# Kernel optimization log

Measured on AMD Instinct MI355X. Metric: run time of the kernel, lower is better.

## Reference

```python
import jax, jax.numpy as jnp
import numpy as np

B, N, C = 32, 577, 768
H = 12
D = C // H


def setup_inputs() -> dict:
    key = jax.random.key(0)
    ks = jax.random.split(key, 4)
    x = jax.random.normal(ks[0], (B, N, C), dtype=jnp.float32)
    w_qkv = jax.random.normal(ks[1], (C, 3 * C), dtype=jnp.float32) * (C ** -0.5)
    b_qkv = jnp.zeros((3 * C,), dtype=jnp.float32)
    # per-head learnable scale, initialized to head_dim**-0.5 scaled ones
    scale = jnp.ones((H,), dtype=jnp.float32) * (D ** -0.5)
    w_proj = jax.random.normal(ks[2], (C, C), dtype=jnp.float32) * (C ** -0.5)
    b_proj = jnp.zeros((C,), dtype=jnp.float32)
    return {"x": x, "w_qkv": w_qkv, "b_qkv": b_qkv, "scale": scale,
            "w_proj": w_proj, "b_proj": b_proj}


def reference(x, w_qkv, b_qkv, scale, w_proj, b_proj):
    b, n, c = x.shape
    h = scale.shape[0]
    d = c // h
    # fused QKV projection -> [b, n, 3, h, d]
    qkv = (x @ w_qkv + b_qkv).reshape(b, n, 3, h, d)
    q = qkv[:, :, 0]  # [b, n, h, d]
    k = qkv[:, :, 1]
    v = qkv[:, :, 2]
    # attention logits with per-head scale
    attn = jnp.einsum('bihd,bjhd->bhij', q, k) * scale[None, :, None, None]
    # custom mask: block self-attention among patch tokens (rows/cols 1:),
    # CLS token (index 0) unaffected
    if n > 1:
        mask = jnp.zeros((n, n), dtype=bool).at[1:, 1:].set(
            jnp.eye(n - 1, dtype=bool))
        attn = jnp.where(mask[None, None], -jnp.inf, attn)
    attn = jax.nn.softmax(attn, axis=-1)
    out = jnp.einsum('bhij,bjhd->bihd', attn, v).reshape(b, n, c)
    return out @ w_proj + b_proj
```

## Files before the change

### kernel.cpp

```cpp
#include <hip/hip_runtime.h>
#include <math.h>

#define HD 64
#define KVBLK 64
#define LP 72

typedef __attribute__((ext_vector_type(8))) short short8;
typedef __attribute__((ext_vector_type(4))) short short4v;
typedef __attribute__((ext_vector_type(4))) float f32x4;

__device__ __forceinline__ short f2bf(float f) {
    union { float f; unsigned u; } in;
    in.f = f;
    unsigned r = (in.u + 0x7fff + ((in.u >> 16) & 1)) >> 16;
    return (short)r;
}

__global__ __launch_bounds__(256) void convert_bf16(const float* __restrict__ in,
                                                    short* __restrict__ out, long n4) {
    long i = blockIdx.x * 256L + threadIdx.x;
    if (i >= n4) return;
    float4 v = reinterpret_cast<const float4*>(in)[i];
    short4v o;
    o[0] = f2bf(v.x); o[1] = f2bf(v.y); o[2] = f2bf(v.z); o[3] = f2bf(v.w);
    reinterpret_cast<short4v*>(out)[i] = o;
}

__global__ __launch_bounds__(256) void transpose_bf16(const float* __restrict__ in,
                                                      short* __restrict__ out, int K, int N) {
    __shared__ float tile[32][33];
    const int n0 = blockIdx.x * 32, k0 = blockIdx.y * 32;
    const int tx = threadIdx.x & 31, ty = threadIdx.x >> 5;
    #pragma unroll
    for (int i = ty; i < 32; i += 8)
        tile[i][tx] = in[(size_t)(k0 + i) * N + n0 + tx];
    __syncthreads();
    #pragma unroll
    for (int i = ty; i < 32; i += 8)
        out[(size_t)(n0 + i) * K + k0 + tx] = f2bf(tile[tx][i]);
}

__global__ __launch_bounds__(256) void transpose_v(const short* __restrict__ qkvb,
                                                   short* __restrict__ vT) {
    constexpr int Nn = 577, C3 = 2304, NH = 12, NKP = 640;
    const int bh = blockIdx.x;
    const int kt = blockIdx.y;
    const int b = bh / NH, h = bh % NH;
    const int tid = threadIdx.x;
    __shared__ short tile[64][33];

    const int tk = tid >> 3;
    const int key = kt * 32 + tk;
    const int d0 = (tid & 7) * 8;
    short8 v = {0, 0, 0, 0, 0, 0, 0, 0};
    if (key < Nn)
        v = *reinterpret_cast<const short8*>(
            qkvb + (size_t)(b * Nn + key) * C3 + 1536 + h * 64 + d0);
    #pragma unroll
    for (int i = 0; i < 8; ++i) tile[d0 + i][tk] = v[i];
    __syncthreads();

    const int d = tid >> 2;
    const int kb = (tid & 3) * 8;
    short8 o;
    #pragma unroll
    for (int i = 0; i < 8; ++i) o[i] = tile[d][kb + i];
    *reinterpret_cast<short8*>(vT + (size_t)(bh * 64 + d) * NKP + kt * 32 + kb) = o;
}

template <typename OutT>
__global__ __launch_bounds__(256, 2) void gemm_bf16(const short* __restrict__ A,
                                                    const short* __restrict__ Bt,
                                                    const float* __restrict__ bias,
                                                    OutT* __restrict__ C,
                                                    int M, int N, int K, int nbn) {
    __shared__ short As[2][128 * 64];
    __shared__ short Bs[2][64 * 64];
    const int tid = threadIdx.x;
    const int w = tid >> 6, lane = tid & 63;
    const int g = lane >> 4, l16 = lane & 15;

    const int nwg = gridDim.x;
    const int q = nwg >> 3, r = nwg & 7;
    const int xcd = blockIdx.x & 7, loc = blockIdx.x >> 3;
    const int wgid = (xcd < r ? xcd * (q + 1) : r * (q + 1) + (xcd - r) * q) + loc;
    const int bm = wgid / nbn, bn = wgid % nbn;
    const int m0 = bm * 256, n0 = bn * 128;
    const int wm = (w >> 1) * 128, wn = (w & 1) * 64;

    f32x4 acc[8][4] = {};
    const int NT = K >> 5;

    auto stage = [&](int buf, int k0) {
        #pragma unroll
        for (int j = 0; j < 4; ++j) {
            const int o = j * 4096 + tid * 16;
            const int R = o >> 7;
            const int sl = ((o >> 4) & 7) ^ (R & 7);
            const int rr = 2 * R + (sl >> 2);
            const int cblk = sl & 3;
            long arow = m0 + rr; if (arow > M - 1) arow = M - 1;
            const short* ga = A + arow * K + k0 + cblk * 8;
            __builtin_amdgcn_global_load_lds(
                (const __attribute__((address_space(1))) unsigned*)ga,
                (__attribute__((address_space(3))) unsigned*)((char*)&As[buf][0] + o),
                16, 0, 0);
        }
        #pragma unroll
        for (int j = 0; j < 2; ++j) {
            const int o = j * 4096 + tid * 16;
            const int R = o >> 7;
            const int sl = ((o >> 4) & 7) ^ (R & 7);
            const int rr = 2 * R + (sl >> 2);
            const int cblk = sl & 3;
            const short* gb = Bt + (size_t)(n0 + rr) * K + k0 + cblk * 8;
            __builtin_amdgcn_global_load_lds(
                (const __attribute__((address_space(1))) unsigned*)gb,
                (__attribute__((address_space(3))) unsigned*)((char*)&Bs[buf][0] + o),
                16, 0, 0);
        }
    };

    stage(0, 0);
    __syncthreads();

    for (int kt = 0; kt < NT; ++kt) {
        const int cur = kt & 1;
        if (kt + 1 < NT) stage(cur ^ 1, (kt + 1) * 32);

        short8 af[8], bfr[4];
        #pragma unroll
        for (int mi = 0; mi < 8; ++mi) {
            const int ra = wm + mi * 16 + l16;
            const int Ra = ra >> 1;
            const int sla = (4 * (ra & 1) + g) ^ (Ra & 7);
            af[mi] = *reinterpret_cast<const short8*>(&As[cur][Ra * 64 + sla * 8]);
        }
        #pragma unroll
        for (int ni = 0; ni < 4; ++ni) {
            const int rb = wn + ni * 16 + l16;
            const int Rb = rb >> 1;
            const int slb = (4 * (rb & 1) + g) ^ (Rb & 7);
            bfr[ni] = *reinterpret_cast<const short8*>(&Bs[cur][Rb * 64 + slb * 8]);
        }
        __builtin_amdgcn_s_setprio(1);
        #pragma unroll
        for (int mi = 0; mi < 8; ++mi)
            #pragma unroll
            for (int ni = 0; ni < 4; ++ni)
                acc[mi][ni] = __builtin_amdgcn_mfma_f32_16x16x32_bf16(
                    af[mi], bfr[ni], acc[mi][ni], 0, 0, 0);
        __builtin_amdgcn_s_setprio(0);
        __syncthreads();
    }

    float bv[4];
    #pragma unroll
    for (int ni = 0; ni < 4; ++ni) bv[ni] = bias[n0 + wn + ni * 16 + l16];
    #pragma unroll
    for (int mi = 0; mi < 8; ++mi) {
        #pragma unroll
        for (int rr = 0; rr < 4; ++rr) {
            const int row = m0 + wm + mi * 16 + g * 4 + rr;
            if (row < M) {
                #pragma unroll
                for (int ni = 0; ni < 4; ++ni) {
                    float val = acc[mi][ni][rr] + bv[ni];
                    if constexpr (__is_same(OutT, float))
                        C[(size_t)row * N + n0 + wn + ni * 16 + l16] = val;
                    else
                        C[(size_t)row * N + n0 + wn + ni * 16 + l16] = f2bf(val);
                }
            }
        }
    }
}

__global__ __launch_bounds__(256) void flash_attn(const short* __restrict__ qkvb,
                                                  const short* __restrict__ vT,
                                                  const float* __restrict__ scale,
                                                  short* __restrict__ out) {
    constexpr int Nn = 577, Cc = 768, C3 = 2304, NQB = 10, NH = 12, NT = 10, NKP = 640;
    const int bid = blockIdx.x;
    const int swz = (bid & 7) * 480 + (bid >> 3);
    const int q0 = (swz % NQB) * 64;
    const int h  = (swz / NQB) % NH;
    const int b  = swz / (NQB * NH);
    const int qblk = q0 >> 6;

    const int tid  = threadIdx.x;
    const int w    = tid >> 6;
    const int lane = tid & 63;
    const int g    = lane >> 4;
    const int l16  = lane & 15;

    __shared__ alignas(16) short Ks[2][KVBLK * HD];
    __shared__ alignas(16) short Vts[2][HD * KVBLK];
    __shared__ alignas(16) short Ps[4][16][LP];

    const float sl2 = scale[h] * 1.44269504088896f;
    const float thr = 8.0f / sl2;
    const short* base = qkvb + (size_t)b * Nn * C3;
    const short* kglob = base + Cc + h * HD;
    const short* vtb = vT + (size_t)(b * NH + h) * HD * NKP;

    const int qrow = q0 + w * 16 + l16;
    const int qr = qrow < Nn ? qrow : Nn - 1;
    const short* qp = base + (size_t)qr * C3 + h * HD;
    short8 aq[2];
    aq[0] = *reinterpret_cast<const short8*>(qp + 8 * g);
    aq[1] = *reinterpret_cast<const short8*>(qp + 32 + 8 * g);

    f32x4 oacc[4] = {};
    float mrun = -INFINITY, m2 = -INFINITY, lrun = 0.f;

    const int kst_row = lane >> 3;
    const int kst_dblk = (lane & 7) ^ (lane >> 3);

    auto stageK = [&](int bufi, int kv0) {
        #pragma unroll
        for (int t = 0; t < 2; ++t) {
            const int i = 2 * w + t;
            int kr = kv0 + 8 * i + kst_row;
            if (kr > Nn - 1) kr = Nn - 1;
            const short* src = kglob + (size_t)kr * C3 + kst_dblk * 8;
            __builtin_amdgcn_global_load_lds(
                (const __attribute__((address_space(1))) unsigned*)src,
                (__attribute__((address_space(3))) unsigned*)&Ks[bufi][i * 512],
                16, 0, 0);
        }
    };
    auto stageV = [&](int bufi, int kv0) {
        #pragma unroll
        for (int t = 0; t < 2; ++t) {
            const int i = 2 * w + t;
            const int r = 8 * i + kst_row;
            const int kb = (lane & 7) ^ (r & 7);
            const short* src = vtb + (size_t)r * NKP + kv0 + kb * 8;
            __builtin_amdgcn_global_load_lds(
                (const __attribute__((address_space(1))) unsigned*)src,
                (__attribute__((address_space(3))) unsigned*)&Vts[bufi][i * 512],
                16, 0, 0);
        }
    };

    stageK(0, 0);
    stageV(0, 0);
    __syncthreads();

    for (int t = 0; t < NT; ++t) {
        const int cur = t & 1, nxt = cur ^ 1;
        const int kv0 = t * KVBLK;
        const bool more = (t + 1 < NT);
        if (more) { stageK(nxt, kv0 + KVBLK); stageV(nxt, kv0 + KVBLK); }

        f32x4 sacc[4] = {};
        __builtin_amdgcn_s_setprio(1);
        #pragma unroll
        for (int f = 0; f < 4; ++f) {
            #pragma unroll
            for (int c = 0; c < 2; ++c) {
                const int slot = (4 * c + g) ^ (l16 & 7);
                short8 ak = *reinterpret_cast<const short8*>(
                    &Ks[cur][(16 * f + l16) * 64 + slot * 8]);
                sacc[f] = __builtin_amdgcn_mfma_f32_16x16x32_bf16(ak, aq[c], sacc[f], 0, 0, 0);
            }
        }
        __builtin_amdgcn_s_setprio(0);

        const int ig = q0 + w * 16 + l16;
        float s2[4][4];
        #pragma unroll
        for (int f = 0; f < 4; ++f)
            #pragma unroll
            for (int r = 0; r < 4; ++r)
                s2[f][r] = sacc[f][r];
        if (t == qblk || t == NT - 1) {
            #pragma unroll
            for (int f = 0; f < 4; ++f)
                #pragma unroll
                for (int r = 0; r < 4; ++r) {
                    const int jg = kv0 + 16 * f + 4 * g + r;
                    if (jg >= Nn || (jg == ig && ig >= 1)) s2[f][r] = -INFINITY;
                }
        }

        float mx = s2[0][0];
        #pragma unroll
        for (int f = 0; f < 4; ++f)
            #pragma unroll
            for (int r = 0; r < 4; ++r)
                if (f + r) mx = fmaxf(mx, s2[f][r]);
        mx = fmaxf(mx, __shfl_xor(mx, 16, 64));
        mx = fmaxf(mx, __shfl_xor(mx, 32, 64));

        if (__any(mx > mrun + thr)) {
            const float mnew = fmaxf(mrun, mx);
            const float m2new = mnew * sl2;
            const float fac = __builtin_amdgcn_exp2f(m2 - m2new);
            mrun = mnew; m2 = m2new;
            lrun *= fac;
            #pragma unroll
            for (int r = 0; r < 4; ++r) {
                const float fr = __shfl(fac, 16 * g + 4 * g + r, 64);
                #pragma unroll
                for (int df = 0; df < 4; ++df) oacc[df][r] *= fr;
            }
        }

        float sum = 0.f;
        #pragma unroll
        for (int f = 0; f < 4; ++f)
            #pragma unroll
            for (int r = 0; r < 4; ++r) {
                float p = __builtin_amdgcn_exp2f(fmaf(s2[f][r], sl2, -m2));
                s2[f][r] = p;
                sum += p;
            }
        sum += __shfl_xor(sum, 16, 64);
        sum += __shfl_xor(sum, 32, 64);
        lrun += sum;

        #pragma unroll
        for (int f = 0; f < 4; ++f) {
            unsigned plo, phi;
            asm("v_cvt_pk_bf16_f32 %0, %1, %2" : "=v"(plo) : "v"(s2[f][0]), "v"(s2[f][1]));
            asm("v_cvt_pk_bf16_f32 %0, %1, %2" : "=v"(phi) : "v"(s2[f][2]), "v"(s2[f][3]));
            unsigned* dst = reinterpret_cast<unsigned*>(&Ps[w][l16][16 * f + 4 * g]);
            dst[0] = plo; dst[1] = phi;
        }
        asm volatile("s_waitcnt lgkmcnt(0)" ::: "memory");

        __builtin_amdgcn_s_setprio(1);
        #pragma unroll
        for (int c = 0; c < 2; ++c) {
            short8 pa = *reinterpret_cast<const short8*>(&Ps[w][l16][32 * c + 8 * g]);
            #pragma unroll
            for (int df = 0; df < 4; ++df) {
                const int slot = (4 * c + g) ^ (l16 & 7);
                short8 bv = *reinterpret_cast<const short8*>(
                    &Vts[cur][(16 * df + l16) * 64 + slot * 8]);
                oacc[df] = __builtin_amdgcn_mfma_f32_16x16x32_bf16(pa, bv, oacc[df], 0, 0, 0);
            }
        }
        __builtin_amdgcn_s_setprio(0);
        __syncthreads();
    }

    #pragma unroll
    for (int r = 0; r < 4; ++r) {
        const int og = q0 + w * 16 + g * 4 + r;
        if (og < Nn) {
            const float lr_r = __shfl(lrun, 16 * g + 4 * g + r, 64);
            const float inv = 1.f / lr_r;
            #pragma unroll
            for (int df = 0; df < 4; ++df)
                out[(size_t)(b * Nn + og) * Cc + h * HD + 16 * df + l16] =
                    f2bf(oacc[df][r] * inv);
        }
    }
}

extern "C" void kernel_launch(void* const* d_in, const int* in_sizes, int n_in,
                              void* d_out, int out_size, void* d_ws, size_t ws_size,
                              hipStream_t stream) {
    const float* x      = (const float*)d_in[0];
    const float* w_qkv  = (const float*)d_in[1];
    const float* b_qkv  = (const float*)d_in[2];
    const float* scale  = (const float*)d_in[3];
    const float* w_proj = (const float*)d_in[4];
    const float* b_proj = (const float*)d_in[5];
    float* out = (float*)d_out;

    const int B = 32, N = 577, C = 768, H = 12;
    const int M  = B * N;
    const int C3 = 3 * C;
    const int MB2 = (M + 255) / 256;

    short* qkvb   = (short*)d_ws;
    short* attn_o = qkvb + (size_t)M * C3;
    short* xb     = attn_o + (size_t)M * C;
    short* wqkvT  = xb + (size_t)M * C;
    short* wprojT = wqkvT + (size_t)C3 * C;
    short* vT     = wprojT + (size_t)C * C;

    dim3 blk(256);
    const long n4 = (long)M * C / 4;
    convert_bf16<<<dim3((n4 + 255) / 256), blk, 0, stream>>>(x, xb, n4);
    transpose_bf16<<<dim3(C3 / 32, C / 32), blk, 0, stream>>>(w_qkv, wqkvT, C, C3);
    transpose_bf16<<<dim3(C / 32, C / 32), blk, 0, stream>>>(w_proj, wprojT, C, C);

    gemm_bf16<short><<<dim3(MB2 * (C3 / 128)), blk, 0, stream>>>(
        xb, wqkvT, b_qkv, qkvb, M, C3, C, C3 / 128);

    transpose_v<<<dim3(B * H, 20), blk, 0, stream>>>(qkvb, vT);

    flash_attn<<<dim3(((N + 63) / 64) * H * B), blk, 0, stream>>>(qkvb, vT, scale, attn_o);

    gemm_bf16<float><<<dim3(MB2 * (C / 128)), blk, 0, stream>>>(
        attn_o, wprojT, b_proj, out, M, C, C, C / 128);
}
```

Before: 247.1 us.

## Fuse V transpose into QKV GEMM epilogue and double flash-attention query tile

Removes the separate transpose_v kernel. The QKV GEMM epilogue now writes the V columns directly into the transposed vT buffer. The flash attention kernel now handles 128 query rows per block, with two 16-row subtiles per wave, so each staged K/V tile is reused twice and the grid is halved. The trade-offs are scattered 2-byte stores in the GEMM epilogue, more registers and shared memory in the attention kernel, and padded key columns in vT that are no longer explicitly zeroed.

```diff
diff --git a/kernel.cpp b/kernel.cpp
--- a/kernel.cpp
+++ b/kernel.cpp
@@ -40,39 +40,12 @@
         out[(size_t)(n0 + i) * K + k0 + tx] = f2bf(tile[tx][i]);
 }
 
-__global__ __launch_bounds__(256) void transpose_v(const short* __restrict__ qkvb,
-                                                   short* __restrict__ vT) {
-    constexpr int Nn = 577, C3 = 2304, NH = 12, NKP = 640;
-    const int bh = blockIdx.x;
-    const int kt = blockIdx.y;
-    const int b = bh / NH, h = bh % NH;
-    const int tid = threadIdx.x;
-    __shared__ short tile[64][33];
-
-    const int tk = tid >> 3;
-    const int key = kt * 32 + tk;
-    const int d0 = (tid & 7) * 8;
-    short8 v = {0, 0, 0, 0, 0, 0, 0, 0};
-    if (key < Nn)
-        v = *reinterpret_cast<const short8*>(
-            qkvb + (size_t)(b * Nn + key) * C3 + 1536 + h * 64 + d0);
-    #pragma unroll
-    for (int i = 0; i < 8; ++i) tile[d0 + i][tk] = v[i];
-    __syncthreads();
-
-    const int d = tid >> 2;
-    const int kb = (tid & 3) * 8;
-    short8 o;
-    #pragma unroll
-    for (int i = 0; i < 8; ++i) o[i] = tile[d][kb + i];
-    *reinterpret_cast<short8*>(vT + (size_t)(bh * 64 + d) * NKP + kt * 32 + kb) = o;
-}
-
-template <typename OutT>
+template <typename OutT, bool WVT>
 __global__ __launch_bounds__(256, 2) void gemm_bf16(const short* __restrict__ A,
                                                     const short* __restrict__ Bt,
                                                     const float* __restrict__ bias,
                                                     OutT* __restrict__ C,
+                                                    short* __restrict__ vT,
                                                     int M, int N, int K, int nbn) {
     __shared__ short As[2][128 * 64];
     __shared__ short Bs[2][64 * 64];
@@ -163,13 +136,23 @@
         for (int rr = 0; rr < 4; ++rr) {
             const int row = m0 + wm + mi * 16 + g * 4 + rr;
             if (row < M) {
-                #pragma unroll
-                for (int ni = 0; ni < 4; ++ni) {
-                    float val = acc[mi][ni][rr] + bv[ni];
-                    if constexpr (__is_same(OutT, float))
-                        C[(size_t)row * N + n0 + wn + ni * 16 + l16] = val;
-                    else
-                        C[(size_t)row * N + n0 + wn + ni * 16 + l16] = f2bf(val);
+                if (WVT && n0 >= 1536) {
+                    const int bb = row / 577, key = row - bb * 577;
+                    #pragma unroll
+                    for (int ni = 0; ni < 4; ++ni) {
+                        const int vcol = n0 + wn + ni * 16 + l16 - 1536;
+                        vT[(size_t)(bb * 768 + vcol) * 640 + key] =
+                            f2bf(acc[mi][ni][rr] + bv[ni]);
+                    }
+                } else {
+                    #pragma unroll
+                    for (int ni = 0; ni < 4; ++ni) {
+                        float val = acc[mi][ni][rr] + bv[ni];
+                        if constexpr (__is_same(OutT, float))
+                            C[(size_t)row * N + n0 + wn + ni * 16 + l16] = val;
+                        else
+                            C[(size_t)row * N + n0 + wn + ni * 16 + l16] = f2bf(val);
+                    }
                 }
             }
         }
@@ -180,13 +163,13 @@
                                                   const short* __restrict__ vT,
                                                   const float* __restrict__ scale,
                                                   short* __restrict__ out) {
-    constexpr int Nn = 577, Cc = 768, C3 = 2304, NQB = 10, NH = 12, NT = 10, NKP = 640;
+    constexpr int Nn = 577, Cc = 768, C3 = 2304, NQB = 5, NH = 12, NT = 10, NKP = 640;
     const int bid = blockIdx.x;
-    const int swz = (bid & 7) * 480 + (bid >> 3);
-    const int q0 = (swz % NQB) * 64;
+    const int swz = (bid & 7) * 240 + (bid >> 3);
+    const int q0 = (swz % NQB) * 128;
     const int h  = (swz / NQB) % NH;
     const int b  = swz / (NQB * NH);
-    const int qblk = q0 >> 6;
+    const int qb2 = q0 >> 6;
 
     const int tid  = threadIdx.x;
     const int w    = tid >> 6;
@@ -196,7 +179,7 @@
 
     __shared__ alignas(16) short Ks[2][KVBLK * HD];
     __shared__ alignas(16) short Vts[2][HD * KVBLK];
-    __shared__ alignas(16) short Ps[4][16][LP];
+    __shared__ alignas(16) short Ps[4][2][16][LP];
 
     const float sl2 = scale[h] * 1.44269504088896f;
     const float thr = 8.0f / sl2;
@@ -204,15 +187,19 @@
     const short* kglob = base + Cc + h * HD;
     const short* vtb = vT + (size_t)(b * NH + h) * HD * NKP;
 
-    const int qrow = q0 + w * 16 + l16;
-    const int qr = qrow < Nn ? qrow : Nn - 1;
-    const short* qp = base + (size_t)qr * C3 + h * HD;
-    short8 aq[2];
-    aq[0] = *reinterpret_cast<const short8*>(qp + 8 * g);
-    aq[1] = *reinterpret_cast<const short8*>(qp + 32 + 8 * g);
-
-    f32x4 oacc[4] = {};
-    float mrun = -INFINITY, m2 = -INFINITY, lrun = 0.f;
+    short8 aq[2][2];
+    #pragma unroll
+    for (int u = 0; u < 2; ++u) {
+        const int qrow = q0 + u * 64 + w * 16 + l16;
+        const int qr = qrow < Nn ? qrow : Nn - 1;
+        const short* qp = base + (size_t)qr * C3 + h * HD;
+        aq[u][0] = *reinterpret_cast<const short8*>(qp + 8 * g);
+        aq[u][1] = *reinterpret_cast<const short8*>(qp + 32 + 8 * g);
+    }
+
+    f32x4 oacc[2][4] = {};
+    float mrun[2] = {-INFINITY, -INFINITY}, m2[2] = {-INFINITY, -INFINITY},
+          lrun[2] = {0.f, 0.f};
 
     const int kst_row = lane >> 3;
     const int kst_dblk = (lane & 7) ^ (lane >> 3);
@@ -254,111 +241,121 @@
         const bool more = (t + 1 < NT);
         if (more) { stageK(nxt, kv0 + KVBLK); stageV(nxt, kv0 + KVBLK); }
 
-        f32x4 sacc[4] = {};
+        f32x4 sacc[2][4] = {};
         __builtin_amdgcn_s_setprio(1);
         #pragma unroll
-        for (int f = 0; f < 4; ++f) {
+        for (int u = 0; u < 2; ++u)
+            #pragma unroll
+            for (int f = 0; f < 4; ++f)
+                #pragma unroll
+                for (int c = 0; c < 2; ++c) {
+                    const int slot = (4 * c + g) ^ (l16 & 7);
+                    short8 ak = *reinterpret_cast<const short8*>(
+                        &Ks[cur][(16 * f + l16) * 64 + slot * 8]);
+                    sacc[u][f] = __builtin_amdgcn_mfma_f32_16x16x32_bf16(
+                        ak, aq[u][c], sacc[u][f], 0, 0, 0);
+                }
+        __builtin_amdgcn_s_setprio(0);
+
+        #pragma unroll
+        for (int u = 0; u < 2; ++u) {
+            const int ig = q0 + u * 64 + w * 16 + l16;
+            float s2[4][4];
+            #pragma unroll
+            for (int f = 0; f < 4; ++f)
+                #pragma unroll
+                for (int r = 0; r < 4; ++r)
+                    s2[f][r] = sacc[u][f][r];
+            if (t == qb2 + u || t == NT - 1) {
+                #pragma unroll
+                for (int f = 0; f < 4; ++f)
+                    #pragma unroll
+                    for (int r = 0; r < 4; ++r) {
+                        const int jg = kv0 + 16 * f + 4 * g + r;
+                        if (jg >= Nn || (jg == ig && ig >= 1)) s2[f][r] = -INFINITY;
+                    }
+            }
+
+            float mx = s2[0][0];
+            #pragma unroll
+            for (int f = 0; f < 4; ++f)
+                #pragma unroll
+                for (int r = 0; r < 4; ++r)
+                    if (f + r) mx = fmaxf(mx, s2[f][r]);
+            mx = fmaxf(mx, __shfl_xor(mx, 16, 64));
+            mx = fmaxf(mx, __shfl_xor(mx, 32, 64));
+
+            if (__any(mx > mrun[u] + thr)) {
+                const float mnew = fmaxf(mrun[u], mx);
+                const float m2new = mnew * sl2;
+                const float fac = __builtin_amdgcn_exp2f(m2[u] - m2new);
+                mrun[u] = mnew; m2[u] = m2new;
+                lrun[u] *= fac;
+                #pragma unroll
+                for (int r = 0; r < 4; ++r) {
+                    const float fr = __shfl(fac, 16 * g + 4 * g + r, 64);
+                    #pragma unroll
+                    for (int df = 0; df < 4; ++df) oacc[u][df][r] *= fr;
+                }
+            }
+
+            float sum = 0.f;
+            #pragma unroll
+            for (int f = 0; f < 4; ++f)
+                #pragma unroll
+                for (int r = 0; r < 4; ++r) {
+                    float p = __builtin_amdgcn_exp2f(fmaf(s2[f][r], sl2, -m2[u]));
+                    s2[f][r] = p;
+                    sum += p;
+                }
+            sum += __shfl_xor(sum, 16, 64);
+            sum += __shfl_xor(sum, 32, 64);
+            lrun[u] += sum;
+
+            #pragma unroll
+            for (int f = 0; f < 4; ++f) {
+                unsigned plo, phi;
+                asm("v_cvt_pk_bf16_f32 %0, %1, %2" : "=v"(plo) : "v"(s2[f][0]), "v"(s2[f][1]));
+                asm("v_cvt_pk_bf16_f32 %0, %1, %2" : "=v"(phi) : "v"(s2[f][2]), "v"(s2[f][3]));
+                unsigned* dst = reinterpret_cast<unsigned*>(&Ps[w][u][l16][16 * f + 4 * g]);
+                dst[0] = plo; dst[1] = phi;
+            }
+        }
+        asm volatile("s_waitcnt lgkmcnt(0)" ::: "memory");
+
+        __builtin_amdgcn_s_setprio(1);
+        #pragma unroll
+        for (int u = 0; u < 2; ++u)
             #pragma unroll
             for (int c = 0; c < 2; ++c) {
-                const int slot = (4 * c + g) ^ (l16 & 7);
-                short8 ak = *reinterpret_cast<const short8*>(
-                    &Ks[cur][(16 * f + l16) * 64 + slot * 8]);
-                sacc[f] = __builtin_amdgcn_mfma_f32_16x16x32_bf16(ak, aq[c], sacc[f], 0, 0, 0);
-            }
-        }
-        __builtin_amdgcn_s_setprio(0);
-
-        const int ig = q0 + w * 16 + l16;
-        float s2[4][4];
-        #pragma unroll
-        for (int f = 0; f < 4; ++f)
-            #pragma unroll
-            for (int r = 0; r < 4; ++r)
-                s2[f][r] = sacc[f][r];
-        if (t == qblk || t == NT - 1) {
-            #pragma unroll
-            for (int f = 0; f < 4; ++f)
-                #pragma unroll
-                for (int r = 0; r < 4; ++r) {
-                    const int jg = kv0 + 16 * f + 4 * g + r;
-                    if (jg >= Nn || (jg == ig && ig >= 1)) s2[f][r] = -INFINITY;
-                }
-        }
-
-        float mx = s2[0][0];
-        #pragma unroll
-        for (int f = 0; f < 4; ++f)
-            #pragma unroll
-            for (int r = 0; r < 4; ++r)
-                if (f + r) mx = fmaxf(mx, s2[f][r]);
-        mx = fmaxf(mx, __shfl_xor(mx, 16, 64));
-        mx = fmaxf(mx, __shfl_xor(mx, 32, 64));
-
-        if (__any(mx > mrun + thr)) {
-            const float mnew = fmaxf(mrun, mx);
-            const float m2new = mnew * sl2;
-            const float fac = __builtin_amdgcn_exp2f(m2 - m2new);
-            mrun = mnew; m2 = m2new;
-            lrun *= fac;
-            #pragma unroll
-            for (int r = 0; r < 4; ++r) {
-                const float fr = __shfl(fac, 16 * g + 4 * g + r, 64);
-                #pragma unroll
-                for (int df = 0; df < 4; ++df) oacc[df][r] *= fr;
-            }
-        }
-
-        float sum = 0.f;
-        #pragma unroll
-        for (int f = 0; f < 4; ++f)
-            #pragma unroll
-            for (int r = 0; r < 4; ++r) {
-                float p = __builtin_amdgcn_exp2f(fmaf(s2[f][r], sl2, -m2));
-                s2[f][r] = p;
-                sum += p;
-            }
-        sum += __shfl_xor(sum, 16, 64);
-        sum += __shfl_xor(sum, 32, 64);
-        lrun += sum;
-
-        #pragma unroll
-        for (int f = 0; f < 4; ++f) {
-            unsigned plo, phi;
-            asm("v_cvt_pk_bf16_f32 %0, %1, %2" : "=v"(plo) : "v"(s2[f][0]), "v"(s2[f][1]));
-            asm("v_cvt_pk_bf16_f32 %0, %1, %2" : "=v"(phi) : "v"(s2[f][2]), "v"(s2[f][3]));
-            unsigned* dst = reinterpret_cast<unsigned*>(&Ps[w][l16][16 * f + 4 * g]);
-            dst[0] = plo; dst[1] = phi;
-        }
-        asm volatile("s_waitcnt lgkmcnt(0)" ::: "memory");
-
-        __builtin_amdgcn_s_setprio(1);
-        #pragma unroll
-        for (int c = 0; c < 2; ++c) {
-            short8 pa = *reinterpret_cast<const short8*>(&Ps[w][l16][32 * c + 8 * g]);
-            #pragma unroll
-            for (int df = 0; df < 4; ++df) {
-                const int slot = (4 * c + g) ^ (l16 & 7);
-                short8 bv = *reinterpret_cast<const short8*>(
-                    &Vts[cur][(16 * df + l16) * 64 + slot * 8]);
-                oacc[df] = __builtin_amdgcn_mfma_f32_16x16x32_bf16(pa, bv, oacc[df], 0, 0, 0);
-            }
-        }
+                short8 pa = *reinterpret_cast<const short8*>(&Ps[w][u][l16][32 * c + 8 * g]);
+                #pragma unroll
+                for (int df = 0; df < 4; ++df) {
+                    const int slot = (4 * c + g) ^ (l16 & 7);
+                    short8 bv = *reinterpret_cast<const short8*>(
+                        &Vts[cur][(16 * df + l16) * 64 + slot * 8]);
+                    oacc[u][df] = __builtin_amdgcn_mfma_f32_16x16x32_bf16(
+                        pa, bv, oacc[u][df], 0, 0, 0);
+                }
+            }
         __builtin_amdgcn_s_setprio(0);
         __syncthreads();
     }
 
     #pragma unroll
-    for (int r = 0; r < 4; ++r) {
-        const int og = q0 + w * 16 + g * 4 + r;
-        if (og < Nn) {
-            const float lr_r = __shfl(lrun, 16 * g + 4 * g + r, 64);
-            const float inv = 1.f / lr_r;
-            #pragma unroll
-            for (int df = 0; df < 4; ++df)
-                out[(size_t)(b * Nn + og) * Cc + h * HD + 16 * df + l16] =
-                    f2bf(oacc[df][r] * inv);
-        }
-    }
+    for (int u = 0; u < 2; ++u)
+        #pragma unroll
+        for (int r = 0; r < 4; ++r) {
+            const int og = q0 + u * 64 + w * 16 + g * 4 + r;
+            if (og < Nn) {
+                const float lr_r = __shfl(lrun[u], 16 * g + 4 * g + r, 64);
+                const float inv = 1.f / lr_r;
+                #pragma unroll
+                for (int df = 0; df < 4; ++df)
+                    out[(size_t)(b * Nn + og) * Cc + h * HD + 16 * df + l16] =
+                        f2bf(oacc[u][df][r] * inv);
+            }
+        }
 }
 
 extern "C" void kernel_launch(void* const* d_in, const int* in_sizes, int n_in,
@@ -390,13 +387,11 @@
     transpose_bf16<<<dim3(C3 / 32, C / 32), blk, 0, stream>>>(w_qkv, wqkvT, C, C3);
     transpose_bf16<<<dim3(C / 32, C / 32), blk, 0, stream>>>(w_proj, wprojT, C, C);
 
-    gemm_bf16<short><<<dim3(MB2 * (C3 / 128)), blk, 0, stream>>>(
-        xb, wqkvT, b_qkv, qkvb, M, C3, C, C3 / 128);
-
-    transpose_v<<<dim3(B * H, 20), blk, 0, stream>>>(qkvb, vT);
-
-    flash_attn<<<dim3(((N + 63) / 64) * H * B), blk, 0, stream>>>(qkvb, vT, scale, attn_o);
-
-    gemm_bf16<float><<<dim3(MB2 * (C / 128)), blk, 0, stream>>>(
-        attn_o, wprojT, b_proj, out, M, C, C, C / 128);
-}
+    gemm_bf16<short, true><<<dim3(MB2 * (C3 / 128)), blk, 0, stream>>>(
+        xb, wqkvT, b_qkv, qkvb, vT, M, C3, C, C3 / 128);
+
+    flash_attn<<<dim3(((N + 127) / 128) * H * B), blk, 0, stream>>>(qkvb, vT, scale, attn_o);
+
+    gemm_bf16<float, false><<<dim3(MB2 * (C / 128)), blk, 0, stream>>>(
+        attn_o, wprojT, b_proj, out, nullptr, M, C, C, C / 128);
+}
```

Result: slower. 263.0 us (+6.4%).
